# Optimization experiments

Hardware: AMD Instinct MI355X
Metric: run time of the kernel (lower is better)

## Reference

```python
import math
import jax, jax.numpy as jnp
import numpy as np

D_MODEL = 1024
N_HEADS = 16
HEAD_DIM = D_MODEL // N_HEADS
ROPE_THETA = 10000.0


def setup_inputs() -> dict:
    key = jax.random.key(0)
    ks = jax.random.split(key, 5)
    B, T = 4, 2048
    # xavier-ish scale for weights
    w_scale = math.sqrt(2.0 / (D_MODEL + D_MODEL))
    return {
        "x": jax.random.normal(ks[0], (B, T, D_MODEL), dtype=jnp.float32),
        "Wq": jax.random.normal(ks[1], (D_MODEL, D_MODEL), dtype=jnp.float32) * w_scale,
        "Wk": jax.random.normal(ks[2], (D_MODEL, D_MODEL), dtype=jnp.float32) * w_scale,
        "Wv": jax.random.normal(ks[3], (D_MODEL, D_MODEL), dtype=jnp.float32) * w_scale,
        "Wo": jax.random.normal(ks[4], (D_MODEL, D_MODEL), dtype=jnp.float32) * w_scale,
    }


def _apply_rope(t, offset=0):
    # t: (B, H, T, Dh); standard half-rotation RoPE
    B, H, T, Dh = t.shape
    inv_freq = 1.0 / (ROPE_THETA ** (jnp.arange(0, Dh, 2, dtype=jnp.float32) / Dh))
    pos = jnp.arange(T, dtype=jnp.float32) + offset  # (T,)
    ang = pos[:, None] * inv_freq[None, :]           # (T, Dh/2)
    cos = jnp.concatenate([jnp.cos(ang), jnp.cos(ang)], axis=-1)  # (T, Dh)
    sin = jnp.concatenate([jnp.sin(ang), jnp.sin(ang)], axis=-1)
    t1, t2 = t[..., : Dh // 2], t[..., Dh // 2 :]
    rot = jnp.concatenate([-t2, t1], axis=-1)
    return t * cos + rot * sin


def _forward(x, Wq, Wk, Wv, Wo):
    B, T, _ = x.shape
    scale = 1.0 / math.sqrt(HEAD_DIM)

    def split_heads(y):  # (B,T,D) -> (B,H,T,Dh)
        return y.reshape(B, T, N_HEADS, HEAD_DIM).transpose(0, 2, 1, 3)

    q = split_heads(x @ Wq.T)
    k = split_heads(x @ Wk.T)
    v = split_heads(x @ Wv.T)

    q = _apply_rope(q)
    k = _apply_rope(k)

    # full materialized scores, as in the original manual SDPA
    scores = jnp.einsum("bhtd,bhsd->bhts", q, k) * scale  # (B,H,T,T)
    causal = jnp.triu(jnp.ones((T, T), dtype=bool), k=1)   # True = masked
    scores = jnp.where(causal[None, None], -jnp.inf, scores)
    attn = jax.nn.softmax(scores, axis=-1)
    attn = jnp.nan_to_num(attn, nan=0.0)
    out = jnp.einsum("bhts,bhsd->bhtd", attn, v)           # (B,H,T,Dh)
    out = out.transpose(0, 2, 1, 3).reshape(B, T, N_HEADS * HEAD_DIM)
    return out @ Wo.T


def reference(x, Wq, Wk, Wv, Wo):
    return _forward(x, Wq, Wk, Wv, Wo)
```

## Files before the change

### kernel.cpp

```cpp
#include <hip/hip_runtime.h>
#include <math.h>

typedef __bf16 bf16_t;
typedef __bf16 bf16x4 __attribute__((ext_vector_type(4)));
typedef __bf16 bf16x8 __attribute__((ext_vector_type(8)));
typedef float f32x4 __attribute__((ext_vector_type(4)));

#define MFMA16(a, b, c) __builtin_amdgcn_mfma_f32_16x16x32_bf16(a, b, c, 0, 0, 0)
#define GLD_LDS16(g, l)                                                                    \
    __builtin_amdgcn_global_load_lds((const __attribute__((address_space(1))) void*)(g),   \
                                     (__attribute__((address_space(3))) void*)(l), 16, 0, 0)

#define SM_SCALE_LOG2E 0.18033688011112042f
#define NEG_LOG2_10K_32 -0.41524101186092029f

__device__ __forceinline__ void fast_sincos(float ang, float* s, float* c) {
    float rev = ang * 0.15915494309189535f;
    rev = rev - floorf(rev);
    *s = __builtin_amdgcn_sinf(rev);
    *c = __builtin_amdgcn_cosf(rev);
}

__global__ void cvt_all(const float* __restrict__ x, const float* __restrict__ wq,
                        const float* __restrict__ wk, const float* __restrict__ wv,
                        const float* __restrict__ wo, bf16_t* __restrict__ out) {
    long i = ((long)blockIdx.x * 256 + threadIdx.x) * 4;
    const float* src;
    long off;
    const long M1 = 1048576;
    if (i < 8 * M1) { src = x;  off = i; }
    else if (i < 9 * M1)  { src = wq; off = i - 8 * M1; }
    else if (i < 10 * M1) { src = wk; off = i - 9 * M1; }
    else if (i < 11 * M1) { src = wv; off = i - 10 * M1; }
    else                  { src = wo; off = i - 11 * M1; }
    float4 v = *(const float4*)(src + off);
    out[i + 0] = (bf16_t)v.x;
    out[i + 1] = (bf16_t)v.y;
    out[i + 2] = (bf16_t)v.z;
    out[i + 3] = (bf16_t)v.w;
}

template <typename OutT>
__global__ __launch_bounds__(256) void gemm_bt(const bf16_t* __restrict__ A,
                                               const bf16_t* __restrict__ B,
                                               OutT* __restrict__ C,
                                               int M, int N, int K) {
    __shared__ __align__(16) bf16_t As[128 * 32];
    __shared__ __align__(16) bf16_t Bs[128 * 32];
    const int tid = threadIdx.x;
    const int lane = tid & 63, wave = tid >> 6;
    const int qd = lane >> 4, ln = lane & 15;
    const int m0 = blockIdx.y * 128, n0 = blockIdx.x * 128;
    const int wr = (wave >> 1) * 64, wc = (wave & 1) * 64;
    const int Kb = K * 2;

    f32x4 acc[4][4];
#pragma unroll
    for (int i = 0; i < 4; ++i)
#pragma unroll
        for (int j = 0; j < 4; ++j)
#pragma unroll
            for (int r = 0; r < 4; ++r) acc[i][j][r] = 0.f;

    const int off0 = wave * 2048 + lane * 16;
    const int off1 = off0 + 1024;
    const int r0 = off0 >> 6, c0 = off0 & 63;
    const int r1 = off1 >> 6, c1 = off1 & 63;

    for (int kt = 0; kt < K; kt += 32) {
        const char* Ab = (const char*)A + (size_t)m0 * Kb + kt * 2;
        const char* Bb = (const char*)B + (size_t)n0 * Kb + kt * 2;
        GLD_LDS16(Ab + (size_t)r0 * Kb + c0, (char*)As + wave * 2048);
        GLD_LDS16(Ab + (size_t)r1 * Kb + c1, (char*)As + wave * 2048 + 1024);
        GLD_LDS16(Bb + (size_t)r0 * Kb + c0, (char*)Bs + wave * 2048);
        GLD_LDS16(Bb + (size_t)r1 * Kb + c1, (char*)Bs + wave * 2048 + 1024);
        __syncthreads();
        bf16x8 af[4], bfr[4];
#pragma unroll
        for (int i = 0; i < 4; ++i)
            af[i] = *(const bf16x8*)(As + (wr + i * 16 + ln) * 32 + qd * 8);
#pragma unroll
        for (int j = 0; j < 4; ++j)
            bfr[j] = *(const bf16x8*)(Bs + (wc + j * 16 + ln) * 32 + qd * 8);
#pragma unroll
        for (int i = 0; i < 4; ++i)
#pragma unroll
            for (int j = 0; j < 4; ++j)
                acc[i][j] = MFMA16(af[i], bfr[j], acc[i][j]);
        __syncthreads();
    }
#pragma unroll
    for (int i = 0; i < 4; ++i)
#pragma unroll
        for (int j = 0; j < 4; ++j)
#pragma unroll
            for (int r = 0; r < 4; ++r) {
                int row = m0 + wr + i * 16 + qd * 4 + r;
                int col = n0 + wc + j * 16 + ln;
                C[(size_t)row * N + col] = (OutT)acc[i][j][r];
            }
}

__global__ __launch_bounds__(256) void gemm_qkv_rope(const bf16_t* __restrict__ A,
                                                     const bf16_t* __restrict__ B,
                                                     bf16_t* __restrict__ Qo,
                                                     bf16_t* __restrict__ Ko,
                                                     bf16_t* __restrict__ Vt,
                                                     int M, int K) {
    __shared__ __align__(16) bf16_t As[128 * 32];
    __shared__ __align__(16) bf16_t Bs[128 * 32];
    const int tid = threadIdx.x;
    const int lane = tid & 63, wave = tid >> 6;
    const int qd = lane >> 4, ln = lane & 15;
    const int m0 = blockIdx.y * 128, n0 = blockIdx.x * 128;
    const int wr = (wave >> 1) * 64, wc = (wave & 1) * 64;
    const int Kb = K * 2;

    f32x4 acc[4][4];
#pragma unroll
    for (int i = 0; i < 4; ++i)
#pragma unroll
        for (int j = 0; j < 4; ++j)
#pragma unroll
            for (int r = 0; r < 4; ++r) acc[i][j][r] = 0.f;

    const int off0 = wave * 2048 + lane * 16;
    const int off1 = off0 + 1024;
    const int r0 = off0 >> 6, c0 = off0 & 63;
    const int r1 = off1 >> 6, c1 = off1 & 63;

    for (int kt = 0; kt < K; kt += 32) {
        const char* Ab = (const char*)A + (size_t)m0 * Kb + kt * 2;
        const char* Bb = (const char*)B + (size_t)n0 * Kb + kt * 2;
        GLD_LDS16(Ab + (size_t)r0 * Kb + c0, (char*)As + wave * 2048);
        GLD_LDS16(Ab + (size_t)r1 * Kb + c1, (char*)As + wave * 2048 + 1024);
        GLD_LDS16(Bb + (size_t)r0 * Kb + c0, (char*)Bs + wave * 2048);
        GLD_LDS16(Bb + (size_t)r1 * Kb + c1, (char*)Bs + wave * 2048 + 1024);
        __syncthreads();
        bf16x8 af[4], bfr[4];
#pragma unroll
        for (int i = 0; i < 4; ++i)
            af[i] = *(const bf16x8*)(As + (wr + i * 16 + ln) * 32 + qd * 8);
#pragma unroll
        for (int j = 0; j < 4; ++j)
            bfr[j] = *(const bf16x8*)(Bs + (wc + j * 16 + ln) * 32 + qd * 8);
#pragma unroll
        for (int i = 0; i < 4; ++i)
#pragma unroll
            for (int j = 0; j < 4; ++j)
                acc[i][j] = MFMA16(af[i], bfr[j], acc[i][j]);
        __syncthreads();
    }

    if (n0 < 2048) {
        const bool isQ = (n0 < 1024);
        bf16_t* Out = isQ ? Qo : Ko;
        const float scale = isQ ? SM_SCALE_LOG2E : 1.0f;
        const int nc0 = n0 & 1023;
        const float inv0 = exp2f((float)ln * NEG_LOG2_10K_32);
        const float inv1 = exp2f((float)(ln + 16) * NEG_LOG2_10K_32);
#pragma unroll
        for (int i = 0; i < 4; ++i) {
#pragma unroll
            for (int r = 0; r < 4; ++r) {
                int row = m0 + wr + i * 16 + qd * 4 + r;
                int t = row & 2047, bb = row >> 11;
                float ft = (float)t;
                float s0, c0v, s1, c1v;
                fast_sincos(ft * inv0, &s0, &c0v);
                fast_sincos(ft * inv1, &s1, &c1v);
#pragma unroll
                for (int j = 0; j < 4; ++j) {
                    int col = nc0 + wc + j * 16 + ln;
                    int h = col >> 6, d = col & 63;
                    float sv = (j & 1) ? s1 : s0;
                    float cv = (j & 1) ? c1v : c0v;
                    float td = acc[i][j][r], tp = acc[i][j ^ 2][r];
                    float o = (j < 2) ? (td * cv - tp * sv) : (td * cv + tp * sv);
                    Out[((size_t)(bb * 16 + h) * 2048 + t) * 64 + d] = (bf16_t)(o * scale);
                }
            }
        }
    } else {
        const int nv0 = n0 - 2048;
#pragma unroll
        for (int i = 0; i < 4; ++i) {
            int tb = m0 + wr + i * 16 + qd * 4;
            int t = tb & 2047, bb = tb >> 11;
#pragma unroll
            for (int j = 0; j < 4; ++j) {
                int col = nv0 + wc + j * 16 + ln;
                int h = col >> 6, d = col & 63;
                bf16x4 pk;
#pragma unroll
                for (int r = 0; r < 4; ++r) pk[r] = (bf16_t)acc[i][j][r];
                *(bf16x4*)(Vt + ((size_t)(bb * 16 + h) * 64 + d) * 2048 + t) = pk;
            }
        }
    }
}

__global__ __launch_bounds__(256) void attn_fwd(const bf16_t* __restrict__ Qg,
                                                const bf16_t* __restrict__ Kg,
                                                const bf16_t* __restrict__ Vtg,
                                                bf16_t* __restrict__ Og) {
    __shared__ __align__(16) bf16_t Kt[64 * 72];
    __shared__ __align__(16) bf16_t Vl[64 * 72];
    __shared__ __align__(16) bf16_t Pl[4][32 * 72];
    const int id = blockIdx.x;
    const int bh = ((id & 7) << 3) | ((id >> 3) & 7);
    const int pair = (id >> 6) & 7;
    const int b = bh >> 4, h = bh & 15;
    const int tid = threadIdx.x, wave = tid >> 6, lane = tid & 63;
    const int qd = lane >> 4, ln = lane & 15;
    const int c0 = tid, c1 = 256 + tid;
    const int kr0r = c0 >> 3, kr0c = (c0 & 7) * 8;
    const int kr1r = c1 >> 3, kr1c = (c1 & 7) * 8;
    const bf16_t* Kbh = Kg + (size_t)bh * 2048 * 64;
    const bf16_t* Vbh = Vtg + (size_t)bh * 64 * 2048;

    bf16x8 vones;
#pragma unroll
    for (int i = 0; i < 8; ++i) vones[i] = (bf16_t)1.0f;

    for (int ph = 0; ph < 2; ++ph) {
        const int qt = ph ? 15 - pair : pair;
        const int q0 = qt * 128;
        const int wrow = q0 + wave * 32;
        const int njt = 2 * qt + 2;

        bf16x8 aq[2][2];
#pragma unroll
        for (int f = 0; f < 2; ++f) {
            const bf16_t* Qbase = Qg + ((size_t)bh * 2048 + wrow + f * 16 + ln) * 64;
            aq[f][0] = *(const bf16x8*)(Qbase + qd * 8);
            aq[f][1] = *(const bf16x8*)(Qbase + 32 + qd * 8);
        }

        f32x4 lsum[2];
        f32x4 o_acc[2][4];
#pragma unroll
        for (int f = 0; f < 2; ++f) {
#pragma unroll
            for (int r = 0; r < 4; ++r) lsum[f][r] = 0.f;
#pragma unroll
            for (int c = 0; c < 4; ++c)
#pragma unroll
                for (int r = 0; r < 4; ++r) o_acc[f][c][r] = 0.f;
        }

        int4 kr0, kr1, vr0, vr1;
        auto issue = [&](int j) {
            const bf16_t* kp = Kbh + (size_t)j * 64 * 64;
            const bf16_t* vp = Vbh + j * 64;
            kr0 = *(const int4*)(kp + kr0r * 64 + kr0c);
            kr1 = *(const int4*)(kp + kr1r * 64 + kr1c);
            vr0 = *(const int4*)(vp + (size_t)kr0r * 2048 + kr0c);
            vr1 = *(const int4*)(vp + (size_t)kr1r * 2048 + kr1c);
        };
        issue(0);

        for (int j = 0; j < njt; ++j) {
            __syncthreads();
            *(int4*)(Kt + kr0r * 72 + kr0c) = kr0;
            *(int4*)(Kt + kr1r * 72 + kr1c) = kr1;
            *(int4*)(Vl + kr0r * 72 + kr0c) = vr0;
            *(int4*)(Vl + kr1r * 72 + kr1c) = vr1;
            __syncthreads();
            if (j + 1 < njt) issue(j + 1);

            if (j * 64 > wrow + 31) continue;
            const int j64 = j * 64;

            f32x4 s[2][4];
#pragma unroll
            for (int st = 0; st < 4; ++st) {
                bf16x8 bk0 = *(const bf16x8*)(Kt + (st * 16 + ln) * 72 + qd * 8);
                bf16x8 bk1 = *(const bf16x8*)(Kt + (st * 16 + ln) * 72 + 32 + qd * 8);
#pragma unroll
                for (int f = 0; f < 2; ++f) {
                    f32x4 t = {0.f, 0.f, 0.f, 0.f};
                    t = MFMA16(aq[f][0], bk0, t);
                    t = MFMA16(aq[f][1], bk1, t);
                    s[f][st] = t;
                }
            }

            if (j64 + 63 <= wrow) {
#pragma unroll
                for (int f = 0; f < 2; ++f)
#pragma unroll
                    for (int st = 0; st < 4; ++st)
#pragma unroll
                        for (int r = 0; r < 4; ++r)
                            s[f][st][r] = __builtin_amdgcn_exp2f(s[f][st][r]);
            } else {
#pragma unroll
                for (int f = 0; f < 2; ++f) {
                    int rowb = wrow + f * 16 + qd * 4;
#pragma unroll
                    for (int st = 0; st < 4; ++st) {
                        int col = j64 + st * 16 + ln;
#pragma unroll
                        for (int r = 0; r < 4; ++r) {
                            float v = (col > rowb + r) ? -INFINITY : s[f][st][r];
                            s[f][st][r] = __builtin_amdgcn_exp2f(v);
                        }
                    }
                }
            }

            bf16_t* P = &Pl[wave][0];
#pragma unroll
            for (int f = 0; f < 2; ++f)
#pragma unroll
                for (int st = 0; st < 4; ++st)
#pragma unroll
                    for (int r = 0; r < 4; ++r)
                        P[(f * 16 + qd * 4 + r) * 72 + st * 16 + ln] = (bf16_t)s[f][st][r];

            bf16x8 bv[4][2];
#pragma unroll
            for (int ct = 0; ct < 4; ++ct) {
                bv[ct][0] = *(const bf16x8*)(Vl + (ct * 16 + ln) * 72 + qd * 8);
                bv[ct][1] = *(const bf16x8*)(Vl + (ct * 16 + ln) * 72 + 32 + qd * 8);
            }
#pragma unroll
            for (int f = 0; f < 2; ++f) {
                bf16x8 ap0 = *(const bf16x8*)(P + (f * 16 + ln) * 72 + qd * 8);
                bf16x8 ap1 = *(const bf16x8*)(P + (f * 16 + ln) * 72 + 32 + qd * 8);
                lsum[f] = MFMA16(ap0, vones, lsum[f]);
                lsum[f] = MFMA16(ap1, vones, lsum[f]);
#pragma unroll
                for (int ct = 0; ct < 4; ++ct) {
                    o_acc[f][ct] = MFMA16(ap0, bv[ct][0], o_acc[f][ct]);
                    o_acc[f][ct] = MFMA16(ap1, bv[ct][1], o_acc[f][ct]);
                }
            }
        }

#pragma unroll
        for (int f = 0; f < 2; ++f) {
            size_t obase = ((size_t)b * 2048 + wrow + f * 16 + qd * 4) * 1024 + h * 64;
            float rl[4];
#pragma unroll
            for (int r = 0; r < 4; ++r) rl[r] = __builtin_amdgcn_rcpf(lsum[f][r]);
#pragma unroll
            for (int ct = 0; ct < 4; ++ct)
#pragma unroll
                for (int r = 0; r < 4; ++r)
                    Og[obase + (size_t)r * 1024 + ct * 16 + ln] =
                        (bf16_t)(o_acc[f][ct][r] * rl[r]);
        }
    }
}

extern "C" void kernel_launch(void* const* d_in, const int* in_sizes, int n_in,
                              void* d_out, int out_size, void* d_ws, size_t ws_size,
                              hipStream_t stream) {
    (void)in_sizes; (void)n_in; (void)out_size; (void)ws_size;
    const float* x  = (const float*)d_in[0];
    const float* Wq = (const float*)d_in[1];
    const float* Wk = (const float*)d_in[2];
    const float* Wv = (const float*)d_in[3];
    const float* Wo = (const float*)d_in[4];
    char* ws = (char*)d_ws;
    const size_t MB = 1ull << 20;
    bf16_t* xb   = (bf16_t*)(ws + 0);
    bf16_t* wqb  = (bf16_t*)(ws + 16 * MB);
    bf16_t* wob  = (bf16_t*)(ws + 22 * MB);
    bf16_t* Qb   = (bf16_t*)(ws + 24 * MB);
    bf16_t* Kb   = (bf16_t*)(ws + 40 * MB);
    bf16_t* Vtb  = (bf16_t*)(ws + 56 * MB);
    bf16_t* AOb  = xb;

    cvt_all<<<dim3(12288), dim3(256), 0, stream>>>(x, Wq, Wk, Wv, Wo, (bf16_t*)ws);

    gemm_qkv_rope<<<dim3(24, 64), dim3(256), 0, stream>>>(xb, wqb, Qb, Kb, Vtb, 8192, 1024);

    attn_fwd<<<dim3(512), dim3(256), 0, stream>>>(Qb, Kb, Vtb, AOb);

    gemm_bt<float><<<dim3(8, 64), dim3(256), 0, stream>>>(AOb, wob, (float*)d_out, 8192, 1024, 1024);
}
```

Baseline: 260.6 us.

## Rewrite QKV+RoPE GEMM as 256x256 double-buffered 8-wave pipelined kernel

Replaces the 128x128, 4-wave, single-buffered QKV projection GEMM with a 256x256 tile, 512-thread kernel. It double-buffers LDS with async global-to-LDS loads that prefetch the next K tile while MFMAs run, and swizzles LDS addresses to avoid bank conflicts. It also raises wave priority around the MFMA bursts. The goals are to hide global-memory latency and to improve operand reuse per load. The cost is a much larger LDS footprint (128 KB) and more registers, which limits occupancy to one block per CU, and the hand-placed waitcnt and barrier choreography is fragile.

```diff
diff --git a/kernel.cpp b/kernel.cpp
--- a/kernel.cpp
+++ b/kernel.cpp
@@ -101,99 +101,178 @@
             }
 }
 
-__global__ __launch_bounds__(256) void gemm_qkv_rope(const bf16_t* __restrict__ A,
-                                                     const bf16_t* __restrict__ B,
-                                                     bf16_t* __restrict__ Qo,
-                                                     bf16_t* __restrict__ Ko,
-                                                     bf16_t* __restrict__ Vt,
-                                                     int M, int K) {
-    __shared__ __align__(16) bf16_t As[128 * 32];
-    __shared__ __align__(16) bf16_t Bs[128 * 32];
+__global__ __launch_bounds__(512) void gemm_qkv_rope8(const bf16_t* __restrict__ A,
+                                                      const bf16_t* __restrict__ B,
+                                                      bf16_t* __restrict__ Qo,
+                                                      bf16_t* __restrict__ Ko,
+                                                      bf16_t* __restrict__ Vt) {
+    __shared__ __align__(16) bf16_t LA[2][2][256 * 32];
+    __shared__ __align__(16) bf16_t LB[2][2][256 * 32];
     const int tid = threadIdx.x;
-    const int lane = tid & 63, wave = tid >> 6;
+    const int wave = tid >> 6, lane = tid & 63;
     const int qd = lane >> 4, ln = lane & 15;
-    const int m0 = blockIdx.y * 128, n0 = blockIdx.x * 128;
-    const int wr = (wave >> 1) * 64, wc = (wave & 1) * 64;
-    const int Kb = K * 2;
-
-    f32x4 acc[4][4];
-#pragma unroll
-    for (int i = 0; i < 4; ++i)
-#pragma unroll
-        for (int j = 0; j < 4; ++j)
-#pragma unroll
-            for (int r = 0; r < 4; ++r) acc[i][j][r] = 0.f;
-
-    const int off0 = wave * 2048 + lane * 16;
-    const int off1 = off0 + 1024;
-    const int r0 = off0 >> 6, c0 = off0 & 63;
-    const int r1 = off1 >> 6, c1 = off1 & 63;
-
-    for (int kt = 0; kt < K; kt += 32) {
-        const char* Ab = (const char*)A + (size_t)m0 * Kb + kt * 2;
-        const char* Bb = (const char*)B + (size_t)n0 * Kb + kt * 2;
-        GLD_LDS16(Ab + (size_t)r0 * Kb + c0, (char*)As + wave * 2048);
-        GLD_LDS16(Ab + (size_t)r1 * Kb + c1, (char*)As + wave * 2048 + 1024);
-        GLD_LDS16(Bb + (size_t)r0 * Kb + c0, (char*)Bs + wave * 2048);
-        GLD_LDS16(Bb + (size_t)r1 * Kb + c1, (char*)Bs + wave * 2048 + 1024);
-        __syncthreads();
-        bf16x8 af[4], bfr[4];
-#pragma unroll
-        for (int i = 0; i < 4; ++i)
-            af[i] = *(const bf16x8*)(As + (wr + i * 16 + ln) * 32 + qd * 8);
-#pragma unroll
-        for (int j = 0; j < 4; ++j)
-            bfr[j] = *(const bf16x8*)(Bs + (wc + j * 16 + ln) * 32 + qd * 8);
-#pragma unroll
-        for (int i = 0; i < 4; ++i)
-#pragma unroll
-            for (int j = 0; j < 4; ++j)
-                acc[i][j] = MFMA16(af[i], bfr[j], acc[i][j]);
-        __syncthreads();
-    }
+    const int wrr = wave >> 2, wcc = wave & 3;
+    const int m0 = blockIdx.y * 256, n0 = blockIdx.x * 256;
+
+    f32x4 acc[8][4];
+#pragma unroll
+    for (int m = 0; m < 8; ++m)
+#pragma unroll
+        for (int n = 0; n < 4; ++n)
+#pragma unroll
+            for (int r = 0; r < 4; ++r) acc[m][n][r] = 0.f;
+
+    const int soff = wave * 1024 + lane * 16;
+    const int slog = soff ^ (((soff >> 7) & 7) << 4);
+    const int srow = slog >> 6;
+    const int scol = slog & 63;
+    const char* Abase = (const char*)A + (size_t)(m0 + srow) * 2048 + scol;
+    const char* Bbase = (const char*)B + (size_t)(n0 + srow) * 2048 + scol;
+
+    int aoff[8], boff[4];
+#pragma unroll
+    for (int m = 0; m < 8; ++m) {
+        int r = m * 32 + wrr * 16 + ln;
+        aoff[m] = ((r << 6) + (qd << 4)) ^ (((r >> 1) & 7) << 4);
+    }
+#pragma unroll
+    for (int n = 0; n < 4; ++n) {
+        int r = wcc * 64 + n * 16 + ln;
+        boff[n] = ((r << 6) + (qd << 4)) ^ (((r >> 1) & 7) << 4);
+    }
+
+    auto stageA = [&](int kt, int kh, int nb) {
+        const char* g = Abase + kt * 128 + kh * 64;
+        char* l = (char*)&LA[nb][kh][0] + wave * 1024;
+        GLD_LDS16(g, l);
+        GLD_LDS16(g + (size_t)128 * 2048, l + 8192);
+    };
+    auto stageB = [&](int kt, int kh, int nb) {
+        const char* g = Bbase + kt * 128 + kh * 64;
+        char* l = (char*)&LB[nb][kh][0] + wave * 1024;
+        GLD_LDS16(g, l);
+        GLD_LDS16(g + (size_t)128 * 2048, l + 8192);
+    };
+
+    bf16x8 fA[4], fB[4];
+#define LOAD_B(kh, bb_)                                          \
+    {                                                            \
+        const char* base_ = (const char*)&LB[bb_][kh][0];        \
+        fB[0] = *(const bf16x8*)(base_ + boff[0]);               \
+        fB[1] = *(const bf16x8*)(base_ + boff[1]);               \
+        fB[2] = *(const bf16x8*)(base_ + boff[2]);               \
+        fB[3] = *(const bf16x8*)(base_ + boff[3]);               \
+    }
+#define LOAD_A(mh, kh, bb_)                                      \
+    {                                                            \
+        const char* base_ = (const char*)&LA[bb_][kh][0];        \
+        fA[0] = *(const bf16x8*)(base_ + aoff[(mh)*4 + 0]);      \
+        fA[1] = *(const bf16x8*)(base_ + aoff[(mh)*4 + 1]);      \
+        fA[2] = *(const bf16x8*)(base_ + aoff[(mh)*4 + 2]);      \
+        fA[3] = *(const bf16x8*)(base_ + aoff[(mh)*4 + 3]);      \
+    }
+#define MFMA_Q(mh)                                                               \
+    {                                                                            \
+        __builtin_amdgcn_s_setprio(1);                                           \
+        _Pragma("unroll") for (int mm = 0; mm < 4; ++mm)                         \
+            _Pragma("unroll") for (int nn = 0; nn < 4; ++nn)                     \
+                acc[(mh)*4 + mm][nn] = MFMA16(fA[mm], fB[nn], acc[(mh)*4 + mm][nn]); \
+        __builtin_amdgcn_s_setprio(0);                                           \
+    }
+#define BAR __builtin_amdgcn_s_barrier()
+#define WAIT_LGKM asm volatile("s_waitcnt lgkmcnt(0)" ::: "memory")
+
+    stageB(0, 0, 0);
+    stageA(0, 0, 0);
+    stageB(0, 1, 0);
+    stageA(0, 1, 0);
+    asm volatile("s_waitcnt vmcnt(4)" ::: "memory");
+    BAR;
+
+    int buf = 0;
+    for (int kt = 0; kt < 16; ++kt) {
+        const int nb = buf ^ 1;
+        const bool pre = (kt + 1 < 16);
+        LOAD_B(0, buf);
+        LOAD_A(0, 0, buf);
+        if (pre) stageB(kt + 1, 0, nb);
+        BAR;
+        WAIT_LGKM;
+        MFMA_Q(0);
+        BAR;
+        LOAD_A(1, 0, buf);
+        if (pre) stageA(kt + 1, 0, nb);
+        BAR;
+        WAIT_LGKM;
+        MFMA_Q(1);
+        if (pre) { asm volatile("s_waitcnt vmcnt(4)" ::: "memory"); }
+        else     { asm volatile("s_waitcnt vmcnt(0)" ::: "memory"); }
+        BAR;
+        LOAD_B(1, buf);
+        LOAD_A(0, 1, buf);
+        if (pre) stageB(kt + 1, 1, nb);
+        BAR;
+        WAIT_LGKM;
+        MFMA_Q(0);
+        BAR;
+        LOAD_A(1, 1, buf);
+        if (pre) stageA(kt + 1, 1, nb);
+        BAR;
+        WAIT_LGKM;
+        MFMA_Q(1);
+        if (pre) { asm volatile("s_waitcnt vmcnt(4)" ::: "memory"); }
+        else     { asm volatile("s_waitcnt vmcnt(0)" ::: "memory"); }
+        BAR;
+        buf = nb;
+    }
+#undef LOAD_B
+#undef LOAD_A
+#undef MFMA_Q
+#undef BAR
+#undef WAIT_LGKM
 
     if (n0 < 2048) {
         const bool isQ = (n0 < 1024);
         bf16_t* Out = isQ ? Qo : Ko;
         const float scale = isQ ? SM_SCALE_LOG2E : 1.0f;
-        const int nc0 = n0 & 1023;
+        const int nc0 = (n0 & 1023) + wcc * 64;
         const float inv0 = exp2f((float)ln * NEG_LOG2_10K_32);
         const float inv1 = exp2f((float)(ln + 16) * NEG_LOG2_10K_32);
 #pragma unroll
-        for (int i = 0; i < 4; ++i) {
+        for (int m = 0; m < 8; ++m) {
 #pragma unroll
             for (int r = 0; r < 4; ++r) {
-                int row = m0 + wr + i * 16 + qd * 4 + r;
+                int row = m0 + m * 32 + wrr * 16 + qd * 4 + r;
                 int t = row & 2047, bb = row >> 11;
                 float ft = (float)t;
                 float s0, c0v, s1, c1v;
                 fast_sincos(ft * inv0, &s0, &c0v);
                 fast_sincos(ft * inv1, &s1, &c1v);
 #pragma unroll
-                for (int j = 0; j < 4; ++j) {
-                    int col = nc0 + wc + j * 16 + ln;
+                for (int n = 0; n < 4; ++n) {
+                    int col = nc0 + n * 16 + ln;
                     int h = col >> 6, d = col & 63;
-                    float sv = (j & 1) ? s1 : s0;
-                    float cv = (j & 1) ? c1v : c0v;
-                    float td = acc[i][j][r], tp = acc[i][j ^ 2][r];
-                    float o = (j < 2) ? (td * cv - tp * sv) : (td * cv + tp * sv);
+                    float sv = (n & 1) ? s1 : s0;
+                    float cv = (n & 1) ? c1v : c0v;
+                    float td = acc[m][n][r], tp = acc[m][n ^ 2][r];
+                    float o = (n < 2) ? (td * cv - tp * sv) : (td * cv + tp * sv);
                     Out[((size_t)(bb * 16 + h) * 2048 + t) * 64 + d] = (bf16_t)(o * scale);
                 }
             }
         }
     } else {
-        const int nv0 = n0 - 2048;
-#pragma unroll
-        for (int i = 0; i < 4; ++i) {
-            int tb = m0 + wr + i * 16 + qd * 4;
+        const int nv0 = (n0 - 2048) + wcc * 64;
+#pragma unroll
+        for (int m = 0; m < 8; ++m) {
+            int tb = m0 + m * 32 + wrr * 16 + qd * 4;
             int t = tb & 2047, bb = tb >> 11;
 #pragma unroll
-            for (int j = 0; j < 4; ++j) {
-                int col = nv0 + wc + j * 16 + ln;
+            for (int n = 0; n < 4; ++n) {
+                int col = nv0 + n * 16 + ln;
                 int h = col >> 6, d = col & 63;
                 bf16x4 pk;
 #pragma unroll
-                for (int r = 0; r < 4; ++r) pk[r] = (bf16_t)acc[i][j][r];
+                for (int r = 0; r < 4; ++r) pk[r] = (bf16_t)acc[m][n][r];
                 *(bf16x4*)(Vt + ((size_t)(bb * 16 + h) * 64 + d) * 2048 + t) = pk;
             }
         }
@@ -376,7 +455,7 @@
 
     cvt_all<<<dim3(12288), dim3(256), 0, stream>>>(x, Wq, Wk, Wv, Wo, (bf16_t*)ws);
 
-    gemm_qkv_rope<<<dim3(24, 64), dim3(256), 0, stream>>>(xb, wqb, Qb, Kb, Vtb, 8192, 1024);
+    gemm_qkv_rope8<<<dim3(12, 32), dim3(512), 0, stream>>>(xb, wqb, Qb, Kb, Vtb);
 
     attn_fwd<<<dim3(512), dim3(256), 0, stream>>>(Qb, Kb, Vtb, AOb);
 
```

After: 260.0 us. Within noise of the previous version (-0.2%).
